# Performance work log

Hardware: AMD Instinct MI355X
Metric: run time of the kernel (lower is better)

## Reference

```python
import jax, jax.numpy as jnp
import numpy as np
import math

SQ, SK, B, NP, HN = 2048, 2048, 2, 16, 128
LAYER_NUM = 1  # coeff
NORM_FACTOR = math.sqrt(2048 / 16) * LAYER_NUM  # sqrt(HIDDEN/HEADS) * coeff
SCALE = float(LAYER_NUM)  # MLSASoftmax scale


def setup_inputs() -> dict:
    key = jax.random.key(0)
    kq, kk, kv = jax.random.split(key, 3)
    query_layer = jax.random.normal(kq, (SQ, B, NP, HN), dtype=jnp.float32)
    key_layer = jax.random.normal(kk, (SK, B, NP, HN), dtype=jnp.float32)
    value_layer = jax.random.normal(kv, (SK, B, NP, HN), dtype=jnp.float32)
    # Causal mask: True = masked, shape [b, 1, sq, sk] (broadcasts over heads)
    causal = jnp.triu(jnp.ones((SQ, SK), dtype=bool), k=1)
    attention_mask = jnp.broadcast_to(causal[None, None], (B, 1, SQ, SK))
    return {
        "query_layer": query_layer,
        "key_layer": key_layer,
        "value_layer": value_layer,
        "attention_mask": attention_mask,
    }


def reference(query_layer, key_layer, value_layer, attention_mask):
    # scores[b,n,s,t] = (Q . K) / norm_factor, then * coeff in softmax
    scores = jnp.einsum("sbnh,tbnh->bnst", query_layer, key_layer) / NORM_FACTOR
    scores = scores * SCALE
    scores = jnp.where(attention_mask, jnp.float32(-10000.0), scores)
    # Module computes exp/sum WITHOUT max-subtraction; replicate exactly.
    exp_mo = jnp.exp(scores)
    denomi = jnp.sum(exp_mo, axis=-1, keepdims=True)  # [b, np, sq, 1]
    probs = exp_mo / denomi
    # dropout is identity in eval / for deterministic baseline
    ctx = jnp.einsum("bnst,tbnh->sbnh", probs, value_layer)  # [sq, b, np, hn]
    sq, b, n, h = ctx.shape
    context_layer = ctx.reshape(sq, b, n * h)
    return (context_layer, denomi)
```

## Files before the change

### kernel.cpp

```cpp
#include <hip/hip_runtime.h>
#include <hip/hip_bf16.h>
#include <stdint.h>

typedef __attribute__((ext_vector_type(8))) short short8;
typedef __attribute__((ext_vector_type(8))) unsigned short ushort8;
typedef __attribute__((ext_vector_type(4))) float f32x4;
typedef __attribute__((ext_vector_type(4))) int int4v;

#define NHEAD 32
#define SEQ   2048
#define HN    128

static constexpr float INV_NORM = 0.08838834764831845f;

__device__ __forceinline__ unsigned short f2bf(float f) {
  union { float f; unsigned u; } v; v.f = f;
  unsigned r = v.u + 0x7fffu + ((v.u >> 16) & 1u);
  return (unsigned short)(r >> 16);
}

__device__ __forceinline__ f32x4 mfma16(short8 a, short8 b, f32x4 c) {
  return __builtin_amdgcn_mfma_f32_16x16x32_bf16(a, b, c, 0, 0, 0);
}

__device__ __forceinline__ void gl_lds16(const void* g, void* l) {
  __builtin_amdgcn_global_load_lds(
      (const __attribute__((address_space(1))) unsigned int*)g,
      (__attribute__((address_space(3))) unsigned int*)l, 16, 0, 0);
}

__global__ __launch_bounds__(256) void prep_kv(const float* __restrict__ K,
                                               const float* __restrict__ V,
                                               unsigned short* __restrict__ kswz,
                                               unsigned short* __restrict__ vT) {
  __shared__ unsigned short lds[128 * 136];
  int bid = blockIdx.x;
  int tid = threadIdx.x;
  if (bid < 4096) {
    int idx = bid * 256 + tid;
    int cl = idx & 15;
    int t  = (idx >> 4) & 2047;
    int bn = idx >> 15;
    const float4* src = (const float4*)(K + ((size_t)t * 32 + bn) * 128 + cl * 8);
    float4 a = src[0], b = src[1];
    ushort8 o;
    o[0]=f2bf(a.x); o[1]=f2bf(a.y); o[2]=f2bf(a.z); o[3]=f2bf(a.w);
    o[4]=f2bf(b.x); o[5]=f2bf(b.y); o[6]=f2bf(b.z); o[7]=f2bf(b.w);
    *(ushort8*)(kswz + ((size_t)bn * 2048 + t) * 128 + ((cl ^ (t & 7)) * 8)) = o;
  } else {
    int vb = bid - 4096;
    int bn = vb >> 4;
    int t0 = (vb & 15) << 7;
    int r = tid >> 1, h0 = (tid & 1) * 64;
    const float* src = V + ((size_t)(t0 + r) * 32 + bn) * 128 + h0;
#pragma unroll
    for (int j = 0; j < 8; ++j) {
      float4 a = *(const float4*)(src + j * 8);
      float4 b = *(const float4*)(src + j * 8 + 4);
      ushort8 o;
      o[0]=f2bf(a.x); o[1]=f2bf(a.y); o[2]=f2bf(a.z); o[3]=f2bf(a.w);
      o[4]=f2bf(b.x); o[5]=f2bf(b.y); o[6]=f2bf(b.z); o[7]=f2bf(b.w);
      *(ushort8*)&lds[r * 136 + h0 + j * 8] = o;
    }
    __syncthreads();
    int h = tid >> 1, ts = (tid & 1) * 64;
    unsigned short tmp[64];
#pragma unroll
    for (int j = 0; j < 64; ++j) {
      int p = j & 31;
      int tloc = ((p >> 3) & 3) * 4 + ((p >> 2) & 1) * 16 + (p & 3);
      tmp[j] = lds[(ts + (j & 32) + tloc) * 136 + h];
    }
    ushort8* dst = (ushort8*)(vT + ((size_t)bn * 128 + h) * 2048 + t0 + ts);
#pragma unroll
    for (int j = 0; j < 8; ++j) dst[j] = *(ushort8*)&tmp[j * 8];
  }
}

template<bool BOTH>
__device__ __forceinline__ void half_tile(
    const char* kb, const char* vbh, int halfbase, int t0h, int qh, int ql,
    int l15, int hi, const short8 (&qf)[2][4],
    f32x4 (&acc)[2][8], float (&dacc)[2]) {
  f32x4 zz = {0.f, 0.f, 0.f, 0.f};
  int xr = (l15 & 7) << 4;
  short8 kf[2][4];
#pragma unroll
  for (int nt = 0; nt < 2; ++nt) {
    const char* krow = kb + (halfbase + nt * 16 + l15) * 256;
#pragma unroll
    for (int kk = 0; kk < 4; ++kk)
      kf[nt][kk] = *(const short8*)(krow + (((kk * 4 + hi) * 16) ^ xr));
  }
  f32x4 sH[2] = {zz, zz}, sL[2] = {zz, zz};
  __builtin_amdgcn_s_setprio(1);
#pragma unroll
  for (int nt = 0; nt < 2; ++nt)
#pragma unroll
    for (int kk = 0; kk < 4; ++kk) {
      sH[nt] = mfma16(kf[nt][kk], qf[0][kk], sH[nt]);
      if (BOTH) sL[nt] = mfma16(kf[nt][kk], qf[1][kk], sL[nt]);
    }
  __builtin_amdgcn_s_setprio(0);
  short8 vf[8];
#pragma unroll
  for (int ht = 0; ht < 8; ++ht)
    vf[ht] = *(const short8*)(vbh + (ht * 16 + l15) * 64 +
                              ((((l15 >> 1) + hi) & 3) * 16));
  auto pack = [&](float (&e)[8], float& da) -> short8 {
    da += ((e[0] + e[1]) + (e[2] + e[3])) + ((e[4] + e[5]) + (e[6] + e[7]));
    unsigned w0, w1, w2, w3;
    asm("v_cvt_pk_bf16_f32 %0, %1, %2" : "=v"(w0) : "v"(e[0]), "v"(e[1]));
    asm("v_cvt_pk_bf16_f32 %0, %1, %2" : "=v"(w1) : "v"(e[2]), "v"(e[3]));
    asm("v_cvt_pk_bf16_f32 %0, %1, %2" : "=v"(w2) : "v"(e[4]), "v"(e[5]));
    asm("v_cvt_pk_bf16_f32 %0, %1, %2" : "=v"(w3) : "v"(e[6]), "v"(e[7]));
    union { int4v u; short8 s; } pk;
    pk.u = (int4v){(int)w0, (int)w1, (int)w2, (int)w3};
    return pk.s;
  };
  auto softp_m = [&](f32x4* sv, int qbase, float& da) -> short8 {
    float e[8];
#pragma unroll
    for (int nt = 0; nt < 2; ++nt)
#pragma unroll
      for (int i = 0; i < 4; ++i) {
        float x = __expf(sv[nt][i] * INV_NORM);
        int kv = t0h + nt * 16 + hi * 4 + i;
        e[nt * 4 + i] = (kv <= qbase + l15) ? x : 0.0f;
      }
    return pack(e, da);
  };
  auto softp_u = [&](f32x4* sv, float& da) -> short8 {
    float e[8];
#pragma unroll
    for (int nt = 0; nt < 2; ++nt)
#pragma unroll
      for (int i = 0; i < 4; ++i)
        e[nt * 4 + i] = __expf(sv[nt][i] * INV_NORM);
    return pack(e, da);
  };
  bool maskH = (t0h + 31 > qh);
  short8 pH = maskH ? softp_m(sH, qh, dacc[0]) : softp_u(sH, dacc[0]);
  short8 pL = {};
  if (BOTH) {
    bool maskL = (t0h + 31 > ql);
    pL = maskL ? softp_m(sL, ql, dacc[1]) : softp_u(sL, dacc[1]);
  }
  __builtin_amdgcn_s_setprio(1);
#pragma unroll
  for (int ht = 0; ht < 8; ++ht) {
    acc[0][ht] = mfma16(pH, vf[ht], acc[0][ht]);
    if (BOTH) acc[1][ht] = mfma16(pL, vf[ht], acc[1][ht]);
  }
  __builtin_amdgcn_s_setprio(0);
}

__global__ __launch_bounds__(256, 2) void attn_main(const float* __restrict__ Q,
                                                    const unsigned short* __restrict__ kswz,
                                                    const unsigned short* __restrict__ vT,
                                                    float* __restrict__ out) {
  __shared__ char smem[65536];
  int tid = threadIdx.x;
  int lane = tid & 63;
  int w = tid >> 6;
  int l15 = lane & 15;
  int hi = lane >> 4;

  int bid = blockIdx.x;
  int bn = bid & 31;
  int x = bid >> 5;
  int p = (x < 8) ? x : 23 - x;
  int qtH = 31 - p, qtL = p;
  int qh = qtH * 64 + w * 16;
  int ql = qtL * 64 + w * 16;
  int ntile = qtH + 1;

  short8 qf[2][4];
#pragma unroll
  for (int qs = 0; qs < 2; ++qs) {
    int qbase = qs ? ql : qh;
    const float* qrow = Q + ((size_t)(qbase + l15) * 32 + bn) * 128;
#pragma unroll
    for (int kk = 0; kk < 4; ++kk) {
      float4 a = *(const float4*)(qrow + kk * 32 + hi * 8);
      float4 b = *(const float4*)(qrow + kk * 32 + hi * 8 + 4);
      short8 o;
      o[0]=(short)f2bf(a.x); o[1]=(short)f2bf(a.y);
      o[2]=(short)f2bf(a.z); o[3]=(short)f2bf(a.w);
      o[4]=(short)f2bf(b.x); o[5]=(short)f2bf(b.y);
      o[6]=(short)f2bf(b.z); o[7]=(short)f2bf(b.w);
      qf[qs][kk] = o;
    }
  }

  f32x4 zz = {0.f, 0.f, 0.f, 0.f};
  f32x4 acc[2][8];
#pragma unroll
  for (int qs = 0; qs < 2; ++qs)
#pragma unroll
    for (int ht = 0; ht < 8; ++ht) acc[qs][ht] = zz;
  float dacc[2] = {0.f, 0.f};

  const char* kg = (const char*)(kswz + (size_t)bn * 2048 * 128);
  const char* vg = (const char*)(vT + (size_t)bn * 128 * 2048);

  auto stage = [&](int buf, int t0) {
    const char* ksrc = kg + (size_t)t0 * 256;
    char* kl = smem + buf * 16384;
    int c = w * 64 + lane;
#pragma unroll
    for (int rr = 0; rr < 4; ++rr)
      gl_lds16(ksrc + (size_t)(c + rr * 256) * 16, kl + (c + rr * 256) * 16);
    char* vl = smem + 32768 + buf * 16384;
#pragma unroll
    for (int s = 0; s < 2; ++s)
#pragma unroll
      for (int rr = 0; rr < 2; ++rr) {
        int c2 = c + rr * 256;
        int h = c2 >> 2, sp = c2 & 3;
        int sl = (sp - (h >> 1)) & 3;
        gl_lds16(vg + (size_t)h * 4096 + (t0 + s * 32) * 2 + sl * 16,
                 vl + s * 8192 + c2 * 16);
      }
  };

  asm volatile("s_waitcnt vmcnt(0)" ::: "memory");
  stage(0, 0);

  int cur = 0;
  for (int it = 0; it < ntile; ++it) {
    int t0 = it * 64;
    asm volatile("s_waitcnt vmcnt(0)" ::: "memory");
    __builtin_amdgcn_s_barrier();
    if (it + 1 < ntile) stage(cur ^ 1, t0 + 64);

    const char* kb = smem + cur * 16384;
    const char* vb = smem + 32768 + cur * 16384;
#pragma unroll
    for (int half = 0; half < 2; ++half) {
      int t0h = t0 + half * 32;
      bool actL = (t0h <= ql + 15);
      bool actH = (t0h <= qh + 15);
      if (actL)
        half_tile<true>(kb, vb + half * 8192, half * 32, t0h, qh, ql,
                        l15, hi, qf, acc, dacc);
      else if (actH)
        half_tile<false>(kb, vb + half * 8192, half * 32, t0h, qh, ql,
                         l15, hi, qf, acc, dacc);
    }
    cur ^= 1;
  }

#pragma unroll
  for (int qs = 0; qs < 2; ++qs) {
    float d = dacc[qs];
    d += __shfl_xor(d, 16);
    d += __shfl_xor(d, 32);
    dacc[qs] = d;
  }
  float* dn = out + 8388608;
  if (hi == 0) {
    dn[(size_t)bn * 2048 + qh + l15] = dacc[0];
    dn[(size_t)bn * 2048 + ql + l15] = dacc[1];
  }
  float invH[4], invL[4];
#pragma unroll
  for (int i = 0; i < 4; ++i) {
    invH[i] = __builtin_amdgcn_rcpf(__shfl(dacc[0], hi * 4 + i));
    invL[i] = __builtin_amdgcn_rcpf(__shfl(dacc[1], hi * 4 + i));
  }

#pragma unroll
  for (int qs = 0; qs < 2; ++qs) {
    int qbase = qs ? ql : qh;
#pragma unroll
    for (int i = 0; i < 4; ++i) {
      float inv = qs ? invL[i] : invH[i];
      float* orow = out + (size_t)(qbase + hi * 4 + i) * 4096 + bn * 128 + l15;
#pragma unroll
      for (int ht = 0; ht < 8; ++ht)
        orow[ht * 16] = acc[qs][ht][i] * inv;
    }
  }
}

extern "C" void kernel_launch(void* const* d_in, const int* in_sizes, int n_in,
                              void* d_out, int out_size, void* d_ws, size_t ws_size,
                              hipStream_t stream) {
  const float* Q = (const float*)d_in[0];
  const float* K = (const float*)d_in[1];
  const float* V = (const float*)d_in[2];
  float* out = (float*)d_out;

  unsigned short* kswz = (unsigned short*)d_ws;
  unsigned short* vT   = kswz + (size_t)NHEAD * SEQ * HN;

  prep_kv<<<4608, 256, 0, stream>>>(K, V, kswz, vT);
  attn_main<<<512, 256, 0, stream>>>(Q, kswz, vT, out);
}
```

Baseline: 82.39 us.

## Assign contiguous 128-row query tiles per block instead of paired high/low tiles

Each block now handles one contiguous 128-row query tile, with each wave owning 32 adjacent rows. Previously a block paired a high and a low 64-row tile to balance causal work. Both 16-row query sub-blocks now share every K/V half-tile, which removes the single-query fallback path and the template specialization. Blocks are ordered longest first to balance the causal workload, though per-block work now varies more than under the pairing scheme. The 1/sqrt(d) scale is folded into Q before the bf16 conversion, removing a multiply per score.

```diff
diff --git a/kernel.cpp b/kernel.cpp
--- a/kernel.cpp
+++ b/kernel.cpp
@@ -77,80 +77,90 @@
   }
 }
 
-template<bool BOTH>
+__device__ __forceinline__ void read_kf(const char* kb, int base, int l15, int hi,
+                                        short8 (&kf)[2][4]) {
+  int xr = (l15 & 7) << 4;
+#pragma unroll
+  for (int nt = 0; nt < 2; ++nt) {
+    const char* krow = kb + (base + nt * 16 + l15) * 256;
+#pragma unroll
+    for (int kk = 0; kk < 4; ++kk)
+      kf[nt][kk] = *(const short8*)(krow + (((kk * 4 + hi) * 16) ^ xr));
+  }
+}
+
+__device__ __forceinline__ void read_vf(const char* vbh, int l15, int hi,
+                                        short8 (&vf)[8]) {
+#pragma unroll
+  for (int ht = 0; ht < 8; ++ht)
+    vf[ht] = *(const short8*)(vbh + (ht * 16 + l15) * 64 +
+                              ((((l15 >> 1) + hi) & 3) * 16));
+}
+
+__device__ __forceinline__ short8 packp(const float (&e)[8], float& da) {
+  da += ((e[0] + e[1]) + (e[2] + e[3])) + ((e[4] + e[5]) + (e[6] + e[7]));
+  unsigned w0, w1, w2, w3;
+  asm("v_cvt_pk_bf16_f32 %0, %1, %2" : "=v"(w0) : "v"(e[0]), "v"(e[1]));
+  asm("v_cvt_pk_bf16_f32 %0, %1, %2" : "=v"(w1) : "v"(e[2]), "v"(e[3]));
+  asm("v_cvt_pk_bf16_f32 %0, %1, %2" : "=v"(w2) : "v"(e[4]), "v"(e[5]));
+  asm("v_cvt_pk_bf16_f32 %0, %1, %2" : "=v"(w3) : "v"(e[6]), "v"(e[7]));
+  union { int4v u; short8 s; } pk;
+  pk.u = (int4v){(int)w0, (int)w1, (int)w2, (int)w3};
+  return pk.s;
+}
+
+__device__ __forceinline__ short8 softp_m(const f32x4 (&sv)[2], int t0h, int qbase,
+                                          int l15, int hi, float& da) {
+  float e[8];
+#pragma unroll
+  for (int nt = 0; nt < 2; ++nt)
+#pragma unroll
+    for (int i = 0; i < 4; ++i) {
+      float x = __expf(sv[nt][i]);
+      int kv = t0h + nt * 16 + hi * 4 + i;
+      e[nt * 4 + i] = (kv <= qbase + l15) ? x : 0.0f;
+    }
+  return packp(e, da);
+}
+
+__device__ __forceinline__ short8 softp_u(const f32x4 (&sv)[2], float& da) {
+  float e[8];
+#pragma unroll
+  for (int nt = 0; nt < 2; ++nt)
+#pragma unroll
+    for (int i = 0; i < 4; ++i)
+      e[nt * 4 + i] = __expf(sv[nt][i]);
+  return packp(e, da);
+}
+
 __device__ __forceinline__ void half_tile(
-    const char* kb, const char* vbh, int halfbase, int t0h, int qh, int ql,
+    const char* kb, const char* vbh, int halfbase, int t0h, int q0, int q1,
     int l15, int hi, const short8 (&qf)[2][4],
     f32x4 (&acc)[2][8], float (&dacc)[2]) {
   f32x4 zz = {0.f, 0.f, 0.f, 0.f};
-  int xr = (l15 & 7) << 4;
   short8 kf[2][4];
-#pragma unroll
-  for (int nt = 0; nt < 2; ++nt) {
-    const char* krow = kb + (halfbase + nt * 16 + l15) * 256;
-#pragma unroll
-    for (int kk = 0; kk < 4; ++kk)
-      kf[nt][kk] = *(const short8*)(krow + (((kk * 4 + hi) * 16) ^ xr));
-  }
-  f32x4 sH[2] = {zz, zz}, sL[2] = {zz, zz};
+  read_kf(kb, halfbase, l15, hi, kf);
+  f32x4 s0[2] = {zz, zz}, s1[2] = {zz, zz};
   __builtin_amdgcn_s_setprio(1);
 #pragma unroll
   for (int nt = 0; nt < 2; ++nt)
 #pragma unroll
     for (int kk = 0; kk < 4; ++kk) {
-      sH[nt] = mfma16(kf[nt][kk], qf[0][kk], sH[nt]);
-      if (BOTH) sL[nt] = mfma16(kf[nt][kk], qf[1][kk], sL[nt]);
+      s0[nt] = mfma16(kf[nt][kk], qf[0][kk], s0[nt]);
+      s1[nt] = mfma16(kf[nt][kk], qf[1][kk], s1[nt]);
     }
   __builtin_amdgcn_s_setprio(0);
   short8 vf[8];
-#pragma unroll
-  for (int ht = 0; ht < 8; ++ht)
-    vf[ht] = *(const short8*)(vbh + (ht * 16 + l15) * 64 +
-                              ((((l15 >> 1) + hi) & 3) * 16));
-  auto pack = [&](float (&e)[8], float& da) -> short8 {
-    da += ((e[0] + e[1]) + (e[2] + e[3])) + ((e[4] + e[5]) + (e[6] + e[7]));
-    unsigned w0, w1, w2, w3;
-    asm("v_cvt_pk_bf16_f32 %0, %1, %2" : "=v"(w0) : "v"(e[0]), "v"(e[1]));
-    asm("v_cvt_pk_bf16_f32 %0, %1, %2" : "=v"(w1) : "v"(e[2]), "v"(e[3]));
-    asm("v_cvt_pk_bf16_f32 %0, %1, %2" : "=v"(w2) : "v"(e[4]), "v"(e[5]));
-    asm("v_cvt_pk_bf16_f32 %0, %1, %2" : "=v"(w3) : "v"(e[6]), "v"(e[7]));
-    union { int4v u; short8 s; } pk;
-    pk.u = (int4v){(int)w0, (int)w1, (int)w2, (int)w3};
-    return pk.s;
-  };
-  auto softp_m = [&](f32x4* sv, int qbase, float& da) -> short8 {
-    float e[8];
-#pragma unroll
-    for (int nt = 0; nt < 2; ++nt)
-#pragma unroll
-      for (int i = 0; i < 4; ++i) {
-        float x = __expf(sv[nt][i] * INV_NORM);
-        int kv = t0h + nt * 16 + hi * 4 + i;
-        e[nt * 4 + i] = (kv <= qbase + l15) ? x : 0.0f;
-      }
-    return pack(e, da);
-  };
-  auto softp_u = [&](f32x4* sv, float& da) -> short8 {
-    float e[8];
-#pragma unroll
-    for (int nt = 0; nt < 2; ++nt)
-#pragma unroll
-      for (int i = 0; i < 4; ++i)
-        e[nt * 4 + i] = __expf(sv[nt][i] * INV_NORM);
-    return pack(e, da);
-  };
-  bool maskH = (t0h + 31 > qh);
-  short8 pH = maskH ? softp_m(sH, qh, dacc[0]) : softp_u(sH, dacc[0]);
-  short8 pL = {};
-  if (BOTH) {
-    bool maskL = (t0h + 31 > ql);
-    pL = maskL ? softp_m(sL, ql, dacc[1]) : softp_u(sL, dacc[1]);
-  }
+  read_vf(vbh, l15, hi, vf);
+  bool m0 = (t0h + 31 > q0);
+  short8 p0 = m0 ? softp_m(s0, t0h, q0, l15, hi, dacc[0]) : softp_u(s0, dacc[0]);
+  bool m1 = (t0h + 31 > q1);
+  short8 p1 = m1 ? softp_m(s1, t0h, q1, l15, hi, dacc[1]) : softp_u(s1, dacc[1]);
   __builtin_amdgcn_s_setprio(1);
 #pragma unroll
   for (int ht = 0; ht < 8; ++ht) {
-    acc[0][ht] = mfma16(pH, vf[ht], acc[0][ht]);
-    if (BOTH) acc[1][ht] = mfma16(pL, vf[ht], acc[1][ht]);
+    acc[0][ht] = mfma16(p0, vf[ht], acc[0][ht]);
+    acc[1][ht] = mfma16(p1, vf[ht], acc[1][ht]);
   }
   __builtin_amdgcn_s_setprio(0);
 }
@@ -168,27 +178,26 @@
 
   int bid = blockIdx.x;
   int bn = bid & 31;
-  int x = bid >> 5;
-  int p = (x < 8) ? x : 23 - x;
-  int qtH = 31 - p, qtL = p;
-  int qh = qtH * 64 + w * 16;
-  int ql = qtL * 64 + w * 16;
-  int ntile = qtH + 1;
+  int z = bid >> 5;
+  int qt = (z < 8) ? (15 - z) : (z - 8);
+  int qb0 = qt * 128 + w * 32;
+  int qb1 = qb0 + 16;
+  int ntile = 2 * qt + 2;
 
   short8 qf[2][4];
 #pragma unroll
   for (int qs = 0; qs < 2; ++qs) {
-    int qbase = qs ? ql : qh;
+    int qbase = qs ? qb1 : qb0;
     const float* qrow = Q + ((size_t)(qbase + l15) * 32 + bn) * 128;
 #pragma unroll
     for (int kk = 0; kk < 4; ++kk) {
       float4 a = *(const float4*)(qrow + kk * 32 + hi * 8);
       float4 b = *(const float4*)(qrow + kk * 32 + hi * 8 + 4);
       short8 o;
-      o[0]=(short)f2bf(a.x); o[1]=(short)f2bf(a.y);
-      o[2]=(short)f2bf(a.z); o[3]=(short)f2bf(a.w);
-      o[4]=(short)f2bf(b.x); o[5]=(short)f2bf(b.y);
-      o[6]=(short)f2bf(b.z); o[7]=(short)f2bf(b.w);
+      o[0]=(short)f2bf(a.x*INV_NORM); o[1]=(short)f2bf(a.y*INV_NORM);
+      o[2]=(short)f2bf(a.z*INV_NORM); o[3]=(short)f2bf(a.w*INV_NORM);
+      o[4]=(short)f2bf(b.x*INV_NORM); o[5]=(short)f2bf(b.y*INV_NORM);
+      o[6]=(short)f2bf(b.z*INV_NORM); o[7]=(short)f2bf(b.w*INV_NORM);
       qf[qs][kk] = o;
     }
   }
@@ -239,14 +248,9 @@
 #pragma unroll
     for (int half = 0; half < 2; ++half) {
       int t0h = t0 + half * 32;
-      bool actL = (t0h <= ql + 15);
-      bool actH = (t0h <= qh + 15);
-      if (actL)
-        half_tile<true>(kb, vb + half * 8192, half * 32, t0h, qh, ql,
-                        l15, hi, qf, acc, dacc);
-      else if (actH)
-        half_tile<false>(kb, vb + half * 8192, half * 32, t0h, qh, ql,
-                         l15, hi, qf, acc, dacc);
+      if (t0h <= qb0)
+        half_tile(kb, vb + half * 8192, half * 32, t0h, qb0, qb1,
+                  l15, hi, qf, acc, dacc);
     }
     cur ^= 1;
   }
@@ -260,22 +264,22 @@
   }
   float* dn = out + 8388608;
   if (hi == 0) {
-    dn[(size_t)bn * 2048 + qh + l15] = dacc[0];
-    dn[(size_t)bn * 2048 + ql + l15] = dacc[1];
-  }
-  float invH[4], invL[4];
+    dn[(size_t)bn * 2048 + qb0 + l15] = dacc[0];
+    dn[(size_t)bn * 2048 + qb1 + l15] = dacc[1];
+  }
+  float inv0[4], inv1[4];
 #pragma unroll
   for (int i = 0; i < 4; ++i) {
-    invH[i] = __builtin_amdgcn_rcpf(__shfl(dacc[0], hi * 4 + i));
-    invL[i] = __builtin_amdgcn_rcpf(__shfl(dacc[1], hi * 4 + i));
+    inv0[i] = __builtin_amdgcn_rcpf(__shfl(dacc[0], hi * 4 + i));
+    inv1[i] = __builtin_amdgcn_rcpf(__shfl(dacc[1], hi * 4 + i));
   }
 
 #pragma unroll
   for (int qs = 0; qs < 2; ++qs) {
-    int qbase = qs ? ql : qh;
+    int qbase = qs ? qb1 : qb0;
 #pragma unroll
     for (int i = 0; i < 4; ++i) {
-      float inv = qs ? invL[i] : invH[i];
+      float inv = qs ? inv1[i] : inv0[i];
       float* orow = out + (size_t)(qbase + hi * 4 + i) * 4096 + bn * 128 + l15;
 #pragma unroll
       for (int ht = 0; ht < 8; ++ht)
```

After: 85.43 us. 3.7% more time.
